# Kernel optimization log

Hardware: AMD Instinct MI355X
Metric: run time of the kernel (lower is better)

Reference implementation:

```python
import jax, jax.numpy as jnp
import numpy as np

H = 8          # query heads
KVH = 4        # key/value heads
D = 256        # head_dim
HID = 2304     # hidden_size
B = 1
S = 4096
SW = 2048      # sliding window
THETA = 10000.0
SCALE = 256 ** -0.5          # query_pre_attn_scalar ** -0.5
SOFTCAP = 50.0
NEG = -1e9


def setup_inputs() -> dict:
    key = jax.random.key(0)
    ks = jax.random.split(key, 6)
    hidden_states = jax.random.normal(ks[0], (B, S, HID), jnp.float32)
    Wq = jax.random.normal(ks[1], (H * D, HID), jnp.float32) * 0.02
    Wk = jax.random.normal(ks[2], (KVH * D, HID), jnp.float32) * 0.02
    Wv = jax.random.normal(ks[3], (KVH * D, HID), jnp.float32) * 0.02
    Wo = jax.random.normal(ks[4], (HID, H * D), jnp.float32) * 0.02
    # causal + sliding-window additive mask: allowed iff 0 <= i-j < SW
    i = jnp.arange(S)[:, None]
    j = jnp.arange(S)[None, :]
    ok = (i >= j) & ((i - j) < SW)
    attention_mask = jnp.where(ok, 0.0, NEG).astype(jnp.float32)[None, None]
    position_ids = jnp.arange(S, dtype=jnp.int32)[None, :]
    return {"hidden_states": hidden_states, "attention_mask": attention_mask,
            "Wq": Wq, "Wk": Wk, "Wv": Wv, "Wo": Wo, "position_ids": position_ids}


def _rope(q, k, position_ids):
    # cos/sin: [B, 1, S, D]
    pos = position_ids.astype(jnp.float32)                      # [B, S]
    inv_freq = 1.0 / (THETA ** (jnp.arange(0, D, 2, dtype=jnp.float32) / D))
    freqs = pos[:, :, None] * inv_freq[None, None, :]           # [B, S, D/2]
    emb = jnp.concatenate([freqs, freqs], axis=-1)              # [B, S, D]
    cos = jnp.cos(emb)[:, None]
    sin = jnp.sin(emb)[:, None]
    rot = lambda x: jnp.concatenate([-x[..., D // 2:], x[..., :D // 2]], axis=-1)
    return q * cos + rot(q) * sin, k * cos + rot(k) * sin


def reference(hidden_states, attention_mask, Wq, Wk, Wv, Wo, position_ids):
    b, s, _ = hidden_states.shape
    q = (hidden_states @ Wq.T).reshape(b, s, H, D).transpose(0, 2, 1, 3)    # [B,H,S,D]
    k = (hidden_states @ Wk.T).reshape(b, s, KVH, D).transpose(0, 2, 1, 3)  # [B,KVH,S,D]
    v = (hidden_states @ Wv.T).reshape(b, s, KVH, D).transpose(0, 2, 1, 3)
    q, k = _rope(q, k, position_ids)
    rep = H // KVH
    k = jnp.repeat(k, rep, axis=1)
    v = jnp.repeat(v, rep, axis=1)
    scores = jnp.einsum('bhqd,bhkd->bhqk', q * SCALE, k)
    scores = jnp.tanh(scores / SOFTCAP) * SOFTCAP + attention_mask
    probs = jax.nn.softmax(scores.astype(jnp.float32), axis=-1).astype(q.dtype)
    out = jnp.einsum('bhqk,bhkd->bhqd', probs, v)
    out = out.transpose(0, 2, 1, 3).reshape(b, s, H * D)
    return out @ Wo.T
```

## Files before the change

kernel.cpp:

```cpp
#include <hip/hip_runtime.h>
#include <hip/hip_bf16.h>
#include <math.h>

#define S 4096
#define HQ 8
#define NKVH 4
#define D 256
#define HID 2304
#define SW 2048
#define QDIM 2048
#define KVDIM 1024
#define QKVDIM 4096
#define SCALE 0.0625f
#define SOFTCAP 50.0f

typedef __attribute__((ext_vector_type(4))) float f32x4;
typedef __attribute__((ext_vector_type(8))) short short8;

__device__ __forceinline__ float bf2f(unsigned v) { return __uint_as_float(v << 16); }
__device__ __forceinline__ unsigned f2bf(float f) {
    unsigned u = __float_as_uint(f);
    return (u + 0x7fffu + ((u >> 16) & 1u)) >> 16;
}

__device__ __forceinline__ void store_c(float* p, float v) { *p = v; }
__device__ __forceinline__ void store_c(unsigned short* p, float v) { *p = (unsigned short)f2bf(v); }

__device__ __forceinline__ void glls16(const void* g, void* l) {
    __builtin_amdgcn_global_load_lds(
        (const __attribute__((address_space(1))) unsigned int*)g,
        (__attribute__((address_space(3))) unsigned int*)l, 16, 0, 0);
}

__global__ __launch_bounds__(256) void cvt_bf16(const float* __restrict__ in,
                                                unsigned short* __restrict__ out)
{
    int i = blockIdx.x * 256 + threadIdx.x;
    float4 v = ((const float4*)in)[i];
    uint2 o;
    o.x = f2bf(v.x) | (f2bf(v.y) << 16);
    o.y = f2bf(v.z) | (f2bf(v.w) << 16);
    ((uint2*)out)[i] = o;
}

template <typename TC>
__global__ __launch_bounds__(256) void bf16_gemm_bt(const unsigned short* __restrict__ A,
                                                    const unsigned short* __restrict__ B,
                                                    TC* __restrict__ C,
                                                    int M, int N, int K)
{
    __shared__ unsigned short As[2][16 * 512];
    __shared__ unsigned short Bs[2][16 * 512];
    const int t = threadIdx.x;

    const int nbx = gridDim.x;
    const int nwg = nbx * gridDim.y;
    int flat = blockIdx.y * nbx + blockIdx.x;
    const int q8 = nwg >> 3, r8 = nwg & 7;
    const int xcd = flat & 7, orig = flat >> 3;
    const int wg = (xcd < r8 ? xcd * (q8 + 1) : r8 * (q8 + 1) + (xcd - r8) * q8) + orig;
    const int band = wg / (8 * nbx);
    const int rem  = wg - band * 8 * nbx;
    const int m0 = (band * 8 + (rem & 7)) * 128;
    const int n0 = (rem >> 3) * 128;

    const int w = t >> 6, lid = t & 63, n16 = lid & 15, quad = lid >> 4;
    const int wm = (w >> 1) * 64, wn = (w & 1) * 64;

    f32x4 acc[4][4] = {};

    auto stage = [&](int buf, int k0) {
        #pragma unroll
        for (int it = 0; it < 4; ++it) {
            int f  = it * 4 + w;
            int fm = f >> 1, fk = f & 1;
            const size_t goff = (size_t)(fm * 16 + n16) * K + k0 + fk * 32 + quad * 8;
            glls16(A + (size_t)m0 * K + goff, &As[buf][f * 512]);
            glls16(B + (size_t)n0 * K + goff, &Bs[buf][f * 512]);
        }
    };

    const int nk = K / 64;
    stage(0, 0);
    int cur = 0;
    for (int kk = 0; kk < nk; ++kk) {
        asm volatile("s_waitcnt vmcnt(0)" ::: "memory");
        __syncthreads();
        if (kk + 1 < nk) stage(cur ^ 1, (kk + 1) * 64);
        #pragma unroll
        for (int ks = 0; ks < 2; ++ks) {
            short8 af[4], bfr[4];
            #pragma unroll
            for (int x = 0; x < 4; ++x) {
                af[x]  = *(const short8*)(&As[cur][(((wm >> 4) + x) * 2 + ks) * 512 + lid * 8]);
                bfr[x] = *(const short8*)(&Bs[cur][(((wn >> 4) + x) * 2 + ks) * 512 + lid * 8]);
            }
            __builtin_amdgcn_s_setprio(1);
            #pragma unroll
            for (int i = 0; i < 4; ++i)
                #pragma unroll
                for (int j = 0; j < 4; ++j)
                    acc[i][j] = __builtin_amdgcn_mfma_f32_16x16x32_bf16(af[i], bfr[j], acc[i][j], 0, 0, 0);
            __builtin_amdgcn_s_setprio(0);
        }
        cur ^= 1;
    }

    #pragma unroll
    for (int i = 0; i < 4; ++i) {
        #pragma unroll
        for (int j = 0; j < 4; ++j) {
            int rbase = m0 + wm + i * 16 + quad * 4;
            int col   = n0 + wn + j * 16 + n16;
            #pragma unroll
            for (int rg = 0; rg < 4; ++rg)
                store_c(C + (size_t)(rbase + rg) * N + col, acc[i][j][rg]);
        }
    }
}

__global__ __launch_bounds__(512, 2) void bf16_gemm_8ph(const unsigned short* __restrict__ A,
                                                        const unsigned short* __restrict__ B,
                                                        unsigned short* __restrict__ C,
                                                        int M, int N, int K)
{
    __shared__ unsigned short As[2][32 * 512];
    __shared__ unsigned short Bs[2][32 * 512];
    const int t = threadIdx.x;
    const int w = t >> 6, lid = t & 63, n16 = lid & 15, quad = lid >> 4;

    const int flat = blockIdx.x;
    const int wg = (flat & 7) * 32 + (flat >> 3);
    const int m0 = (wg >> 4) * 256, n0 = (wg & 15) * 256;

    const int wmf = (w >> 2) * 8;
    const int wnf = (w & 3) * 4;
    const int fnw = (w >> 1) * 4 + (w & 1);

    f32x4 acc[8][4] = {};

    auto stageA = [&](int buf, int k0, int fm) {
        glls16(A + (size_t)(m0 + fm * 16 + n16) * K + k0 + quad * 8,
               &As[buf][(fm * 2 + 0) * 512]);
        glls16(A + (size_t)(m0 + fm * 16 + n16) * K + k0 + 32 + quad * 8,
               &As[buf][(fm * 2 + 1) * 512]);
    };
    auto stageB = [&](int buf, int k0, int fn) {
        glls16(B + (size_t)(n0 + fn * 16 + n16) * K + k0 + quad * 8,
               &Bs[buf][(fn * 2 + 0) * 512]);
        glls16(B + (size_t)(n0 + fn * 16 + n16) * K + k0 + 32 + quad * 8,
               &Bs[buf][(fn * 2 + 1) * 512]);
    };
    auto sAm0 = [&](int buf, int k0){ stageA(buf, k0, (w & 3) + (w >> 2) * 8); };
    auto sAm1 = [&](int buf, int k0){ stageA(buf, k0, 4 + (w & 3) + (w >> 2) * 8); };
    auto sBn0 = [&](int buf, int k0){ stageB(buf, k0, fnw); };
    auto sBn1 = [&](int buf, int k0){ stageB(buf, k0, fnw + 2); };

#define GPHASE(mh, nh, buf, STAGE, WAITSTR)                                          \
    {                                                                                \
        short8 afr[4][2], bfr[2][2];                                                 \
        _Pragma("unroll") for (int i = 0; i < 4; ++i)                                \
            _Pragma("unroll") for (int ks = 0; ks < 2; ++ks)                         \
                afr[i][ks] = *(const short8*)(&As[buf][((wmf + (mh)*4 + i)*2 + ks)*512 + lid*8]); \
        _Pragma("unroll") for (int j = 0; j < 2; ++j)                                \
            _Pragma("unroll") for (int ks = 0; ks < 2; ++ks)                         \
                bfr[j][ks] = *(const short8*)(&Bs[buf][((wnf + (nh)*2 + j)*2 + ks)*512 + lid*8]); \
        STAGE;                                                                       \
        __builtin_amdgcn_s_barrier();                                                \
        asm volatile("s_waitcnt lgkmcnt(0)" ::: "memory");                           \
        __builtin_amdgcn_sched_barrier(0);                                           \
        __builtin_amdgcn_s_setprio(1);                                               \
        _Pragma("unroll") for (int i = 0; i < 4; ++i)                                \
            _Pragma("unroll") for (int j = 0; j < 2; ++j)                            \
                _Pragma("unroll") for (int ks = 0; ks < 2; ++ks)                     \
                    acc[(mh)*4 + i][(nh)*2 + j] = __builtin_amdgcn_mfma_f32_16x16x32_bf16( \
                        afr[i][ks], bfr[j][ks], acc[(mh)*4 + i][(nh)*2 + j], 0, 0, 0); \
        __builtin_amdgcn_s_setprio(0);                                               \
        asm volatile(WAITSTR ::: "memory");                                          \
        __builtin_amdgcn_s_barrier();                                                \
    }

    const int nk = K / 64;
    const int niter = nk / 2;

    sAm0(0, 0); sBn0(0, 0); sAm1(0, 0); sBn1(0, 0);
    sAm0(1, 64); sBn0(1, 64);
    asm volatile("s_waitcnt vmcnt(4)" ::: "memory");
    __builtin_amdgcn_s_barrier();

    for (int I = 0; I < niter - 1; ++I) {
        const int kc = I * 128;
        GPHASE(0, 0, 0, sAm1(1, kc + 64);,  "")
        GPHASE(0, 1, 0, sBn1(1, kc + 64);,  "")
        GPHASE(1, 0, 0, sAm0(0, kc + 128);, "")
        GPHASE(1, 1, 0, sBn0(0, kc + 128);, "s_waitcnt vmcnt(4)")
        GPHASE(0, 0, 1, sAm1(0, kc + 128);, "")
        GPHASE(0, 1, 1, sBn1(0, kc + 128);, "")
        GPHASE(1, 0, 1, sAm0(1, kc + 192);, "")
        GPHASE(1, 1, 1, sBn0(1, kc + 192);, "s_waitcnt vmcnt(4)")
    }
    {
        const int kc = (niter - 1) * 128;
        GPHASE(0, 0, 0, sAm1(1, kc + 64);, "")
        GPHASE(0, 1, 0, sBn1(1, kc + 64);, "")
        GPHASE(1, 0, 0, {};,               "")
        GPHASE(1, 1, 0, {};,               "s_waitcnt vmcnt(0)")
        GPHASE(0, 0, 1, {};,               "")
        GPHASE(0, 1, 1, {};,               "")
        GPHASE(1, 0, 1, {};,               "")
        GPHASE(1, 1, 1, {};,               "")
    }
#undef GPHASE

    #pragma unroll
    for (int mi = 0; mi < 8; ++mi) {
        #pragma unroll
        for (int nj = 0; nj < 4; ++nj) {
            int rbase = m0 + (w >> 2) * 128 + mi * 16 + quad * 4;
            int col   = n0 + (w & 3) * 64 + nj * 16 + n16;
            #pragma unroll
            for (int rg = 0; rg < 4; ++rg)
                store_c(C + (size_t)(rbase + rg) * N + col, acc[mi][nj][rg]);
        }
    }
}

__global__ __launch_bounds__(256) void rope_kernel(const unsigned short* __restrict__ QKV,
                                                   unsigned short* __restrict__ Qb,
                                                   unsigned short* __restrict__ Kb,
                                                   const int* __restrict__ pos_ids)
{
    int id   = blockIdx.x * 256 + threadIdx.x;
    int d    = id & 127;
    int rest = id >> 7;
    int hh   = rest % 12;
    int i    = rest / 12;
    float pos = (float)pos_ids[i];
    float inv = __expf((float)d * (-9.210340371976184f / 128.0f));
    float ang = pos * inv;
    float sn, cs;
    sincosf(ang, &sn, &cs);
    if (hh < HQ) {
        const unsigned short* p = QKV + (size_t)i * QKVDIM + hh * D + d;
        float x0 = bf2f(p[0]), x1 = bf2f(p[128]);
        unsigned short* q = Qb + (size_t)i * QDIM + hh * D + d;
        q[0]   = (unsigned short)f2bf((x0 * cs - x1 * sn) * SCALE);
        q[128] = (unsigned short)f2bf((x1 * cs + x0 * sn) * SCALE);
    } else {
        const unsigned short* p = QKV + (size_t)i * QKVDIM + QDIM + (hh - HQ) * D + d;
        float x0 = bf2f(p[0]), x1 = bf2f(p[128]);
        unsigned short* k = Kb + (size_t)i * KVDIM + (hh - HQ) * D + d;
        k[0]   = (unsigned short)f2bf(x0 * cs - x1 * sn);
        k[128] = (unsigned short)f2bf(x1 * cs + x0 * sn);
    }
}

__global__ __launch_bounds__(256) void transpose_v(const unsigned short* __restrict__ QKV,
                                                   unsigned short* __restrict__ Vt)
{
    __shared__ float tile[64][65];
    const int s0 = blockIdx.x * 64, d0 = blockIdx.y * 64;
    const int t = threadIdx.x;
    #pragma unroll
    for (int it = 0; it < 4; ++it) {
        int flat = it * 256 + t;
        int r  = flat >> 4;
        int c4 = (flat & 15) * 4;
        uint2 v = *(const uint2*)(QKV + (size_t)(s0 + r) * QKVDIM + (QDIM + KVDIM) + d0 + c4);
        tile[r][c4 + 0] = bf2f(v.x & 0xffffu); tile[r][c4 + 1] = bf2f(v.x >> 16);
        tile[r][c4 + 2] = bf2f(v.y & 0xffffu); tile[r][c4 + 3] = bf2f(v.y >> 16);
    }
    __syncthreads();
    #pragma unroll
    for (int it = 0; it < 4; ++it) {
        int flat = it * 256 + t;
        int dr  = flat >> 4;
        int sc4 = (flat & 15) * 4;
        uint2 o;
        o.x = f2bf(tile[sc4 + 0][dr]) | (f2bf(tile[sc4 + 1][dr]) << 16);
        o.y = f2bf(tile[sc4 + 2][dr]) | (f2bf(tile[sc4 + 3][dr]) << 16);
        *(uint2*)(Vt + (size_t)(d0 + dr) * S + s0 + sc4) = o;
    }
}

__global__ __launch_bounds__(256, 2) void attn_kernel(const unsigned short* __restrict__ Qb,
                                                      const unsigned short* __restrict__ Kb,
                                                      const unsigned short* __restrict__ Vt,
                                                      unsigned short* __restrict__ O)
{
    __shared__ unsigned short Ks[32 * 512];
    __shared__ unsigned short Vs[32 * 512];
    __shared__ unsigned short Ps[4 * 1024];
    const int t = threadIdx.x;
    const int bid = blockIdx.x;
    const int b2 = bid & 255;
    const int h = b2 & 7, kvh = h >> 1;
    const int u = b2 >> 3;
    const int g = (bid < 256) ? u : 63 - u;
    const int i0 = g * 64;
    const int w = t >> 6, lid = t & 63, n16 = lid & 15, quad = lid >> 4;
    const int qbase = i0 + w * 16;
    unsigned short* Pw = Ps + w * 1024;

    const unsigned short* Kbase = Kb + kvh * D + quad * 8;
    const unsigned short* Vbase = Vt + (size_t)(kvh * D + n16) * S + quad * 8;

    uint4 kr0, kr1, kr2, kr3, kr4, kr5, kr6, kr7;
    uint4 vr0, vr1, vr2, vr3, vr4, vr5, vr6, vr7;

#define KADDR(J0, IT) (Kbase + (size_t)((J0) + (((IT)*4 + w) >> 3) * 16 + n16) * KVDIM + (((IT)*4 + w) & 7) * 32)
#define VADDR(J0, IT) (Vbase + (size_t)((((IT)*4 + w) >> 1) * 16) * S + (J0) + (((IT)*4 + w) & 1) * 32)
#define ISSUE(J0) do { const int _j = (J0);                                   \
        kr0 = *(const uint4*)KADDR(_j, 0); kr1 = *(const uint4*)KADDR(_j, 1); \
        kr2 = *(const uint4*)KADDR(_j, 2); kr3 = *(const uint4*)KADDR(_j, 3); \
        kr4 = *(const uint4*)KADDR(_j, 4); kr5 = *(const uint4*)KADDR(_j, 5); \
        kr6 = *(const uint4*)KADDR(_j, 6); kr7 = *(const uint4*)KADDR(_j, 7); \
        vr0 = *(const uint4*)VADDR(_j, 0); vr1 = *(const uint4*)VADDR(_j, 1); \
        vr2 = *(const uint4*)VADDR(_j, 2); vr3 = *(const uint4*)VADDR(_j, 3); \
        vr4 = *(const uint4*)VADDR(_j, 4); vr5 = *(const uint4*)VADDR(_j, 5); \
        vr6 = *(const uint4*)VADDR(_j, 6); vr7 = *(const uint4*)VADDR(_j, 7); \
    } while (0)
#define COMMIT() do {                                                          \
        *(uint4*)(&Ks[(0*4 + w) * 512 + lid * 8]) = kr0;                       \
        *(uint4*)(&Ks[(1*4 + w) * 512 + lid * 8]) = kr1;                       \
        *(uint4*)(&Ks[(2*4 + w) * 512 + lid * 8]) = kr2;                       \
        *(uint4*)(&Ks[(3*4 + w) * 512 + lid * 8]) = kr3;                       \
        *(uint4*)(&Ks[(4*4 + w) * 512 + lid * 8]) = kr4;                       \
        *(uint4*)(&Ks[(5*4 + w) * 512 + lid * 8]) = kr5;                       \
        *(uint4*)(&Ks[(6*4 + w) * 512 + lid * 8]) = kr6;                       \
        *(uint4*)(&Ks[(7*4 + w) * 512 + lid * 8]) = kr7;                       \
        *(uint4*)(&Vs[(0*4 + w) * 512 + lid * 8]) = vr0;                       \
        *(uint4*)(&Vs[(1*4 + w) * 512 + lid * 8]) = vr1;                       \
        *(uint4*)(&Vs[(2*4 + w) * 512 + lid * 8]) = vr2;                       \
        *(uint4*)(&Vs[(3*4 + w) * 512 + lid * 8]) = vr3;                       \
        *(uint4*)(&Vs[(4*4 + w) * 512 + lid * 8]) = vr4;                       \
        *(uint4*)(&Vs[(5*4 + w) * 512 + lid * 8]) = vr5;                       \
        *(uint4*)(&Vs[(6*4 + w) * 512 + lid * 8]) = vr6;                       \
        *(uint4*)(&Vs[(7*4 + w) * 512 + lid * 8]) = vr7;                       \
    } while (0)

    short8 qf[8];
    #pragma unroll
    for (int ks = 0; ks < 8; ++ks)
        qf[ks] = *(const short8*)(Qb + (size_t)(qbase + n16) * QDIM + h * D + ks * 32 + quad * 8);

    float lacc[4] = {0.f, 0.f, 0.f, 0.f};
    f32x4 Oacc[16] = {};

    const int jt_min = (i0 >= SW) ? ((i0 - (SW - 1)) >> 6) : 0;
    const int jt_max = (i0 + 63) >> 6;

    ISSUE(jt_min * 64);

    for (int jt = jt_min; jt <= jt_max; ++jt) {
        const int j0 = jt * 64;
        asm volatile("s_waitcnt vmcnt(0)" ::: "memory");
        COMMIT();
        __syncthreads();
        if (jt < jt_max) ISSUE((jt + 1) * 64);

        f32x4 sc[4] = {};
        __builtin_amdgcn_s_setprio(1);
        #pragma unroll
        for (int ks = 0; ks < 8; ++ks) {
            #pragma unroll
            for (int nt = 0; nt < 4; ++nt) {
                short8 kf = *(const short8*)(&Ks[(nt * 8 + ks) * 512 + lid * 8]);
                sc[nt] = __builtin_amdgcn_mfma_f32_16x16x32_bf16(qf[ks], kf, sc[nt], 0, 0, 0);
            }
        }
        __builtin_amdgcn_s_setprio(0);

        #pragma unroll
        for (int nt = 0; nt < 4; ++nt) {
            int j = j0 + nt * 16 + n16;
            #pragma unroll
            for (int rg = 0; rg < 4; ++rg) {
                int iq = qbase + quad * 4 + rg;
                float e = __expf(sc[nt][rg] * (2.0f / SOFTCAP));
                float p = __expf(-100.0f * __builtin_amdgcn_rcpf(e + 1.0f));
                bool ok = (j <= iq) && (iq - j < SW);
                p = ok ? p : 0.0f;
                lacc[rg] += p;
                Pw[(nt >> 1) * 512 + (quad * 4 + rg + 16 * ((nt & 1) * 2 + (n16 >> 3))) * 8 + (n16 & 7)]
                    = (unsigned short)f2bf(p);
            }
        }

        asm volatile("s_waitcnt lgkmcnt(0)" ::: "memory");

        short8 pf0 = *(const short8*)(Pw + lid * 8);
        short8 pf1 = *(const short8*)(Pw + 512 + lid * 8);
        __builtin_amdgcn_s_setprio(1);
        #pragma unroll
        for (int dt = 0; dt < 16; ++dt) {
            short8 vf0 = *(const short8*)(&Vs[(dt * 2 + 0) * 512 + lid * 8]);
            Oacc[dt] = __builtin_amdgcn_mfma_f32_16x16x32_bf16(pf0, vf0, Oacc[dt], 0, 0, 0);
            short8 vf1 = *(const short8*)(&Vs[(dt * 2 + 1) * 512 + lid * 8]);
            Oacc[dt] = __builtin_amdgcn_mfma_f32_16x16x32_bf16(pf1, vf1, Oacc[dt], 0, 0, 0);
        }
        __builtin_amdgcn_s_setprio(0);

        __syncthreads();
    }
#undef KADDR
#undef VADDR
#undef ISSUE
#undef COMMIT

    float linv[4];
    #pragma unroll
    for (int rg = 0; rg < 4; ++rg) {
        float rs = lacc[rg];
        rs += __shfl_xor(rs, 1); rs += __shfl_xor(rs, 2);
        rs += __shfl_xor(rs, 4); rs += __shfl_xor(rs, 8);
        linv[rg] = 1.0f / rs;
    }
    #pragma unroll
    for (int dt = 0; dt < 16; ++dt) {
        int col = h * D + dt * 16 + n16;
        #pragma unroll
        for (int rg = 0; rg < 4; ++rg) {
            int row = qbase + quad * 4 + rg;
            O[(size_t)row * QDIM + col] = (unsigned short)f2bf(Oacc[dt][rg] * linv[rg]);
        }
    }
}

extern "C" void kernel_launch(void* const* d_in, const int* in_sizes, int n_in,
                              void* d_out, int out_size, void* d_ws, size_t ws_size,
                              hipStream_t stream) {
    const float* hidden = (const float*)d_in[0];
    const float* Wq = (const float*)d_in[2];
    const float* Wk = (const float*)d_in[3];
    const float* Wv = (const float*)d_in[4];
    const float* Wo = (const float*)d_in[5];
    const int* pos = (const int*)d_in[6];
    float* out = (float*)d_out;

    char* ws = (char*)d_ws;
    unsigned short* Hb   = (unsigned short*)(ws);
    unsigned short* Qb   = (unsigned short*)(ws);
    unsigned short* Wqkv = (unsigned short*)(ws + (size_t)(18 << 20));
    unsigned short* QKVf = (unsigned short*)(ws + (size_t)(37 << 20));
    unsigned short* Oa   = (unsigned short*)(ws + (size_t)(37 << 20));
    unsigned short* Kb   = (unsigned short*)(ws + (size_t)(69 << 20));
    unsigned short* Vt   = (unsigned short*)(ws + (size_t)(77 << 20));

    cvt_bf16<<<(S * HID) / 1024, 256, 0, stream>>>(hidden, Hb);
    cvt_bf16<<<(QDIM * HID) / 1024, 256, 0, stream>>>(Wq, Wqkv);
    cvt_bf16<<<(KVDIM * HID) / 1024, 256, 0, stream>>>(Wk, Wqkv + (size_t)QDIM * HID);
    cvt_bf16<<<(KVDIM * HID) / 1024, 256, 0, stream>>>(Wv, Wqkv + (size_t)(QDIM + KVDIM) * HID);

    bf16_gemm_8ph<<<256, 512, 0, stream>>>(Hb, Wqkv, QKVf, S, QKVDIM, HID);

    rope_kernel<<<(S * 12 * 128) / 256, 256, 0, stream>>>(QKVf, Qb, Kb, pos);
    transpose_v<<<dim3(S / 64, KVDIM / 64), 256, 0, stream>>>(QKVf, Vt);

    attn_kernel<<<512, 256, 0, stream>>>(Qb, Kb, Vt, Oa);

    cvt_bf16<<<(HID * QDIM) / 1024, 256, 0, stream>>>(Wo, Wqkv);
    bf16_gemm_bt<float><<<dim3(HID / 128, S / 128), 256, 0, stream>>>(Oa, Wqkv, out, S, HID, QDIM);
}
```

Before: 553.7 us.

## Reuse 8-phase 256x256 GEMM for output projection and share LDS fragment reads

```diff
diff --git a/kernel.cpp b/kernel.cpp
--- a/kernel.cpp
+++ b/kernel.cpp
@@ -44,100 +44,29 @@
 }
 
 template <typename TC>
-__global__ __launch_bounds__(256) void bf16_gemm_bt(const unsigned short* __restrict__ A,
-                                                    const unsigned short* __restrict__ B,
-                                                    TC* __restrict__ C,
-                                                    int M, int N, int K)
-{
-    __shared__ unsigned short As[2][16 * 512];
-    __shared__ unsigned short Bs[2][16 * 512];
-    const int t = threadIdx.x;
-
-    const int nbx = gridDim.x;
-    const int nwg = nbx * gridDim.y;
-    int flat = blockIdx.y * nbx + blockIdx.x;
-    const int q8 = nwg >> 3, r8 = nwg & 7;
-    const int xcd = flat & 7, orig = flat >> 3;
-    const int wg = (xcd < r8 ? xcd * (q8 + 1) : r8 * (q8 + 1) + (xcd - r8) * q8) + orig;
-    const int band = wg / (8 * nbx);
-    const int rem  = wg - band * 8 * nbx;
-    const int m0 = (band * 8 + (rem & 7)) * 128;
-    const int n0 = (rem >> 3) * 128;
-
-    const int w = t >> 6, lid = t & 63, n16 = lid & 15, quad = lid >> 4;
-    const int wm = (w >> 1) * 64, wn = (w & 1) * 64;
-
-    f32x4 acc[4][4] = {};
-
-    auto stage = [&](int buf, int k0) {
-        #pragma unroll
-        for (int it = 0; it < 4; ++it) {
-            int f  = it * 4 + w;
-            int fm = f >> 1, fk = f & 1;
-            const size_t goff = (size_t)(fm * 16 + n16) * K + k0 + fk * 32 + quad * 8;
-            glls16(A + (size_t)m0 * K + goff, &As[buf][f * 512]);
-            glls16(B + (size_t)n0 * K + goff, &Bs[buf][f * 512]);
-        }
-    };
-
-    const int nk = K / 64;
-    stage(0, 0);
-    int cur = 0;
-    for (int kk = 0; kk < nk; ++kk) {
-        asm volatile("s_waitcnt vmcnt(0)" ::: "memory");
-        __syncthreads();
-        if (kk + 1 < nk) stage(cur ^ 1, (kk + 1) * 64);
-        #pragma unroll
-        for (int ks = 0; ks < 2; ++ks) {
-            short8 af[4], bfr[4];
-            #pragma unroll
-            for (int x = 0; x < 4; ++x) {
-                af[x]  = *(const short8*)(&As[cur][(((wm >> 4) + x) * 2 + ks) * 512 + lid * 8]);
-                bfr[x] = *(const short8*)(&Bs[cur][(((wn >> 4) + x) * 2 + ks) * 512 + lid * 8]);
-            }
-            __builtin_amdgcn_s_setprio(1);
-            #pragma unroll
-            for (int i = 0; i < 4; ++i)
-                #pragma unroll
-                for (int j = 0; j < 4; ++j)
-                    acc[i][j] = __builtin_amdgcn_mfma_f32_16x16x32_bf16(af[i], bfr[j], acc[i][j], 0, 0, 0);
-            __builtin_amdgcn_s_setprio(0);
-        }
-        cur ^= 1;
-    }
-
-    #pragma unroll
-    for (int i = 0; i < 4; ++i) {
-        #pragma unroll
-        for (int j = 0; j < 4; ++j) {
-            int rbase = m0 + wm + i * 16 + quad * 4;
-            int col   = n0 + wn + j * 16 + n16;
-            #pragma unroll
-            for (int rg = 0; rg < 4; ++rg)
-                store_c(C + (size_t)(rbase + rg) * N + col, acc[i][j][rg]);
-        }
-    }
-}
-
 __global__ __launch_bounds__(512, 2) void bf16_gemm_8ph(const unsigned short* __restrict__ A,
                                                         const unsigned short* __restrict__ B,
-                                                        unsigned short* __restrict__ C,
-                                                        int M, int N, int K)
+                                                        TC* __restrict__ C,
+                                                        int M, int N, int K, int nbn)
 {
     __shared__ unsigned short As[2][32 * 512];
     __shared__ unsigned short Bs[2][32 * 512];
     const int t = threadIdx.x;
     const int w = t >> 6, lid = t & 63, n16 = lid & 15, quad = lid >> 4;
 
+    const int nwg = gridDim.x;
     const int flat = blockIdx.x;
-    const int wg = (flat & 7) * 32 + (flat >> 3);
-    const int m0 = (wg >> 4) * 256, n0 = (wg & 15) * 256;
+    const int wg = (flat & 7) * (nwg >> 3) + (flat >> 3);
+    const int m0 = (wg / nbn) * 256, n0 = (wg % nbn) * 256;
 
     const int wmf = (w >> 2) * 8;
     const int wnf = (w & 3) * 4;
     const int fnw = (w >> 1) * 4 + (w & 1);
 
     f32x4 acc[8][4] = {};
+    short8 afr[4][2];
+    short8 bfr0[2][2];
+    short8 bfr1[2][2];
 
     auto stageA = [&](int buf, int k0, int fm) {
         glls16(A + (size_t)(m0 + fm * 16 + n16) * K + k0 + quad * 8,
@@ -156,15 +85,17 @@
     auto sBn0 = [&](int buf, int k0){ stageB(buf, k0, fnw); };
     auto sBn1 = [&](int buf, int k0){ stageB(buf, k0, fnw + 2); };
 
-#define GPHASE(mh, nh, buf, STAGE, WAITSTR)                                          \
+#define RD_A(mh, buf)                                                                \
+    _Pragma("unroll") for (int i = 0; i < 4; ++i)                                    \
+        _Pragma("unroll") for (int ks = 0; ks < 2; ++ks)                             \
+            afr[i][ks] = *(const short8*)(&As[buf][((wmf + (mh)*4 + i)*2 + ks)*512 + lid*8]);
+#define RD_B(dst, nh, buf)                                                           \
+    _Pragma("unroll") for (int j = 0; j < 2; ++j)                                    \
+        _Pragma("unroll") for (int ks = 0; ks < 2; ++ks)                             \
+            dst[j][ks] = *(const short8*)(&Bs[buf][((wnf + (nh)*2 + j)*2 + ks)*512 + lid*8]);
+
+#define GPHASE(mh, nh, BFR, STAGE, WAITSTR)                                          \
     {                                                                                \
-        short8 afr[4][2], bfr[2][2];                                                 \
-        _Pragma("unroll") for (int i = 0; i < 4; ++i)                                \
-            _Pragma("unroll") for (int ks = 0; ks < 2; ++ks)                         \
-                afr[i][ks] = *(const short8*)(&As[buf][((wmf + (mh)*4 + i)*2 + ks)*512 + lid*8]); \
-        _Pragma("unroll") for (int j = 0; j < 2; ++j)                                \
-            _Pragma("unroll") for (int ks = 0; ks < 2; ++ks)                         \
-                bfr[j][ks] = *(const short8*)(&Bs[buf][((wnf + (nh)*2 + j)*2 + ks)*512 + lid*8]); \
         STAGE;                                                                       \
         __builtin_amdgcn_s_barrier();                                                \
         asm volatile("s_waitcnt lgkmcnt(0)" ::: "memory");                           \
@@ -174,7 +105,7 @@
             _Pragma("unroll") for (int j = 0; j < 2; ++j)                            \
                 _Pragma("unroll") for (int ks = 0; ks < 2; ++ks)                     \
                     acc[(mh)*4 + i][(nh)*2 + j] = __builtin_amdgcn_mfma_f32_16x16x32_bf16( \
-                        afr[i][ks], bfr[j][ks], acc[(mh)*4 + i][(nh)*2 + j], 0, 0, 0); \
+                        afr[i][ks], BFR[j][ks], acc[(mh)*4 + i][(nh)*2 + j], 0, 0, 0); \
         __builtin_amdgcn_s_setprio(0);                                               \
         asm volatile(WAITSTR ::: "memory");                                          \
         __builtin_amdgcn_s_barrier();                                                \
@@ -190,27 +121,41 @@
 
     for (int I = 0; I < niter - 1; ++I) {
         const int kc = I * 128;
-        GPHASE(0, 0, 0, sAm1(1, kc + 64);,  "")
-        GPHASE(0, 1, 0, sBn1(1, kc + 64);,  "")
-        GPHASE(1, 0, 0, sAm0(0, kc + 128);, "")
-        GPHASE(1, 1, 0, sBn0(0, kc + 128);, "s_waitcnt vmcnt(4)")
-        GPHASE(0, 0, 1, sAm1(0, kc + 128);, "")
-        GPHASE(0, 1, 1, sBn1(0, kc + 128);, "")
-        GPHASE(1, 0, 1, sAm0(1, kc + 192);, "")
-        GPHASE(1, 1, 1, sBn0(1, kc + 192);, "s_waitcnt vmcnt(4)")
+        RD_A(0, 0) RD_B(bfr0, 0, 0)
+        GPHASE(0, 0, bfr0, sAm1(1, kc + 64);,  "")
+        RD_B(bfr1, 1, 0)
+        GPHASE(0, 1, bfr1, sBn1(1, kc + 64);,  "")
+        RD_A(1, 0)
+        GPHASE(1, 0, bfr0, sAm0(0, kc + 128);, "")
+        GPHASE(1, 1, bfr1, sBn0(0, kc + 128);, "s_waitcnt vmcnt(4)")
+        RD_A(0, 1) RD_B(bfr0, 0, 1)
+        GPHASE(0, 0, bfr0, sAm1(0, kc + 128);, "")
+        RD_B(bfr1, 1, 1)
+        GPHASE(0, 1, bfr1, sBn1(0, kc + 128);, "")
+        RD_A(1, 1)
+        GPHASE(1, 0, bfr0, sAm0(1, kc + 192);, "")
+        GPHASE(1, 1, bfr1, sBn0(1, kc + 192);, "s_waitcnt vmcnt(4)")
     }
     {
         const int kc = (niter - 1) * 128;
-        GPHASE(0, 0, 0, sAm1(1, kc + 64);, "")
-        GPHASE(0, 1, 0, sBn1(1, kc + 64);, "")
-        GPHASE(1, 0, 0, {};,               "")
-        GPHASE(1, 1, 0, {};,               "s_waitcnt vmcnt(0)")
-        GPHASE(0, 0, 1, {};,               "")
-        GPHASE(0, 1, 1, {};,               "")
-        GPHASE(1, 0, 1, {};,               "")
-        GPHASE(1, 1, 1, {};,               "")
+        RD_A(0, 0) RD_B(bfr0, 0, 0)
+        GPHASE(0, 0, bfr0, sAm1(1, kc + 64);, "")
+        RD_B(bfr1, 1, 0)
+        GPHASE(0, 1, bfr1, sBn1(1, kc + 64);, "")
+        RD_A(1, 0)
+        GPHASE(1, 0, bfr0, {};,               "")
+        GPHASE(1, 1, bfr1, {};,               "s_waitcnt vmcnt(0)")
+        RD_A(0, 1) RD_B(bfr0, 0, 1)
+        GPHASE(0, 0, bfr0, {};,               "")
+        RD_B(bfr1, 1, 1)
+        GPHASE(0, 1, bfr1, {};,               "")
+        RD_A(1, 1)
+        GPHASE(1, 0, bfr0, {};,               "")
+        GPHASE(1, 1, bfr1, {};,               "")
     }
 #undef GPHASE
+#undef RD_A
+#undef RD_B
 
     #pragma unroll
     for (int mi = 0; mi < 8; ++mi) {
@@ -452,7 +397,7 @@
     cvt_bf16<<<(KVDIM * HID) / 1024, 256, 0, stream>>>(Wk, Wqkv + (size_t)QDIM * HID);
     cvt_bf16<<<(KVDIM * HID) / 1024, 256, 0, stream>>>(Wv, Wqkv + (size_t)(QDIM + KVDIM) * HID);
 
-    bf16_gemm_8ph<<<256, 512, 0, stream>>>(Hb, Wqkv, QKVf, S, QKVDIM, HID);
+    bf16_gemm_8ph<unsigned short><<<256, 512, 0, stream>>>(Hb, Wqkv, QKVf, S, QKVDIM, HID, 16);
 
     rope_kernel<<<(S * 12 * 128) / 256, 256, 0, stream>>>(QKVf, Qb, Kb, pos);
     transpose_v<<<dim3(S / 64, KVDIM / 64), 256, 0, stream>>>(QKVf, Vt);
@@ -460,5 +405,5 @@
     attn_kernel<<<512, 256, 0, stream>>>(Qb, Kb, Vt, Oa);
 
     cvt_bf16<<<(HID * QDIM) / 1024, 256, 0, stream>>>(Wo, Wqkv);
-    bf16_gemm_bt<float><<<dim3(HID / 128, S / 128), 256, 0, stream>>>(Oa, Wqkv, out, S, HID, QDIM);
-}
+    bf16_gemm_8ph<float><<<144, 512, 0, stream>>>(Oa, Wqkv, out, S, HID, QDIM, 9);
+}
```

New measurement: 496.2 us. 10.4% less time.
